# Performance work log

Hardware: AMD Instinct MI355X
Metric: run time of the kernel (lower is better)

## Reference

```python
import jax, jax.numpy as jnp
import numpy as np
import math

N_EMBD = 1024
NUM_HEADS = 16
HEAD_DIM = N_EMBD // NUM_HEADS


def alibi_slopes(num_heads):
    x = (2 ** 8) ** (1.0 / num_heads)
    return jnp.array([1.0 / x ** (i + 1) for i in range(num_heads)], dtype=jnp.float32)


def setup_inputs() -> dict:
    key = jax.random.key(0)
    k1, k2 = jax.random.split(key)
    x = jax.random.normal(k1, (2, 2048, N_EMBD), dtype=jnp.float32)
    W_kqv = jax.random.normal(k2, (3 * N_EMBD, N_EMBD), dtype=jnp.float32) * (1.0 / math.sqrt(N_EMBD))
    return {"x": x, "W_kqv": W_kqv}


def reference(x, W_kqv):
    B, S, E = x.shape
    H, D = NUM_HEADS, HEAD_DIM
    kqv = jnp.einsum('bse,fe->bsf', x, W_kqv)  # Linear without bias
    k, q, v = jnp.split(kqv, 3, axis=-1)       # chunk order: key, query, value
    # [B, H, S, D]
    q = q.reshape(B, S, H, D).transpose(0, 2, 1, 3)
    k = k.reshape(B, S, H, D).transpose(0, 2, 1, 3)
    v = v.reshape(B, S, H, D).transpose(0, 2, 1, 3)
    # ALiBi bias: slopes[h] * (j - i), shape [H, S, S]
    rel = jnp.arange(S)[None, :] - jnp.arange(S)[:, None]  # [S, S]
    bias = alibi_slopes(H)[:, None, None] * rel.astype(jnp.float32)
    scale = math.sqrt(E)  # NOTE: module scales by sqrt(n_embd), not sqrt(head_dim)
    score = jnp.einsum('bhqd,bhkd->bhqk', q, k) / scale + bias[None]
    causal = jnp.tril(jnp.ones((S, S), dtype=bool))
    score = jnp.where(causal[None, None], score, -jnp.inf)
    attn = jax.nn.softmax(score, axis=-1)
    out = jnp.einsum('bhqk,bhkd->bhqd', attn, v)
    return out.transpose(0, 2, 1, 3).reshape(B, S, E)
```

## Files before the change

### kernel.cpp

```cpp
#include <hip/hip_runtime.h>
#include <hip/hip_bf16.h>
#include <math.h>

#define TOTAL_B 2
#define SEQ 2048
#define EMB 1024
#define NH 16
#define HD 64
#define M_GEMM (TOTAL_B*SEQ)
#define N_GEMM (3*EMB)
#define K_GEMM EMB

typedef __attribute__((ext_vector_type(8))) short short8;
typedef __attribute__((ext_vector_type(4))) float f32x4;
typedef __attribute__((ext_vector_type(4))) unsigned u32x4;

static __device__ __forceinline__ short f2bf(float f) {
  union { float f; unsigned u; } v; v.f = f;
  unsigned r = v.u + 0x7fff + ((v.u >> 16) & 1u);
  return (short)(r >> 16);
}

static __device__ __forceinline__ void gload_lds16(const void* g, void* l) {
  __builtin_amdgcn_global_load_lds(
      (const __attribute__((address_space(1))) void*)(uintptr_t)g,
      (__attribute__((address_space(3))) void*)(uintptr_t)l, 16, 0, 0);
}

static __device__ __forceinline__ float exp2v(float x) {
  float r; asm("v_exp_f32 %0, %1" : "=v"(r) : "v"(x)); return r;
}
static __device__ __forceinline__ unsigned cvtpk(float lo, float hi) {
  unsigned r; asm("v_cvt_pk_bf16_f32 %0, %1, %2" : "=v"(r) : "v"(lo), "v"(hi)); return r;
}
static __device__ __forceinline__ void pl32swap(unsigned &a, unsigned &b) {
  asm("v_permlane32_swap_b32 %0, %1" : "+v"(a), "+v"(b));
}

__global__ void cvt_kernel(const float* __restrict__ x, const float* __restrict__ w,
                           short* __restrict__ xb, short* __restrict__ wb) {
  const long nx = (long)M_GEMM * K_GEMM;
  const long nw = (long)N_GEMM * K_GEMM;
  long i = (long)blockIdx.x * blockDim.x + threadIdx.x;
  const long tot = (nx + nw) / 8;
  if (i >= tot) return;
  long e = i * 8;
  const float* s; short* d;
  if (e < nx) { s = x + e; d = xb + e; }
  else        { s = w + (e - nx); d = wb + (e - nx); }
  float4 a = ((const float4*)s)[0];
  float4 b = ((const float4*)s)[1];
  short8 o;
  o[0]=f2bf(a.x); o[1]=f2bf(a.y); o[2]=f2bf(a.z); o[3]=f2bf(a.w);
  o[4]=f2bf(b.x); o[5]=f2bf(b.y); o[6]=f2bf(b.z); o[7]=f2bf(b.w);
  *(short8*)d = o;
}

__global__ __launch_bounds__(512, 2) void qkv_gemm(const short* __restrict__ A, const short* __restrict__ Bm,
                                                   short* __restrict__ Kb, short* __restrict__ Qb,
                                                   short* __restrict__ Vb) {
  __shared__ __align__(16) short lds[57344];
  const int tid = threadIdx.x;
  const int lane = tid & 63;
  const int wid = tid >> 6;
  const int lr = lane & 15, lg = lane >> 4;
  const int m0 = blockIdx.y * 256, n0 = blockIdx.x * 192;
  const int wr = wid >> 1;
  const int wc = wid & 1;
  const int srcRow = tid >> 3;
  const int srcCh  = (tid & 7) ^ (srcRow & 7);

  f32x4 acc[4][6] = {};

  auto stageA = [&](int buf, int kt, int u) {
    const int row = u*64 + srcRow;
    gload_lds16(A + (size_t)(m0 + row)*K_GEMM + kt*64 + srcCh*8,
                &lds[buf*16384 + u*4096 + tid*8]);
  };
  auto stageB = [&](int buf, int kt, int u) {
    const int row = u*64 + srcRow;
    gload_lds16(Bm + (size_t)(n0 + row)*K_GEMM + kt*64 + srcCh*8,
                &lds[32768 + buf*12288 + u*4096 + tid*8]);
  };
  auto readA = [&](int buf, int mi, int kk) -> short8 {
    const int r = wr*64 + mi*16 + lr;
    const int c = (kk*4 + lg) ^ (r & 7);
    return *(const short8*)(&lds[buf*16384 + r*64 + c*8]);
  };
  auto readB = [&](int buf, int nj, int kk) -> short8 {
    const int r = wc*96 + nj*16 + lr;
    const int c = (kk*4 + lg) ^ (r & 7);
    return *(const short8*)(&lds[32768 + buf*12288 + r*64 + c*8]);
  };

#pragma unroll
  for (int u = 0; u < 4; ++u) stageA(0, 0, u);
#pragma unroll
  for (int u = 0; u < 3; ++u) stageB(0, 0, u);
  asm volatile("s_waitcnt vmcnt(0)" ::: "memory");
  __builtin_amdgcn_s_barrier();

  short8 aq[2][2], bq[6][2];
  const int NT = K_GEMM / 64;
#pragma unroll 1
  for (int kt = 0; kt < NT; ++kt) {
    const int buf = kt & 1, nb = buf ^ 1;
    const bool more = (kt + 1 < NT);

#pragma unroll
    for (int kk = 0; kk < 2; ++kk) {
      aq[0][kk] = readA(buf, 0, kk); aq[1][kk] = readA(buf, 1, kk);
      bq[0][kk] = readB(buf, 0, kk); bq[1][kk] = readB(buf, 1, kk); bq[2][kk] = readB(buf, 2, kk);
    }
    if (more) { stageA(nb, kt+1, 0); stageA(nb, kt+1, 1); }
    __builtin_amdgcn_s_barrier();
    asm volatile("s_waitcnt lgkmcnt(0)" ::: "memory");
    __builtin_amdgcn_sched_barrier(0);
    __builtin_amdgcn_s_setprio(1);
#pragma unroll
    for (int mi = 0; mi < 2; ++mi)
#pragma unroll
      for (int nj = 0; nj < 3; ++nj)
#pragma unroll
        for (int kk = 0; kk < 2; ++kk)
          acc[mi][nj] = __builtin_amdgcn_mfma_f32_16x16x32_bf16(aq[mi][kk], bq[nj][kk], acc[mi][nj], 0, 0, 0);
    __builtin_amdgcn_s_setprio(0);
    __builtin_amdgcn_sched_barrier(0);
    __builtin_amdgcn_s_barrier();

#pragma unroll
    for (int kk = 0; kk < 2; ++kk) {
      bq[3][kk] = readB(buf, 3, kk); bq[4][kk] = readB(buf, 4, kk); bq[5][kk] = readB(buf, 5, kk);
    }
    if (more) { stageA(nb, kt+1, 2); stageA(nb, kt+1, 3); }
    __builtin_amdgcn_s_barrier();
    asm volatile("s_waitcnt lgkmcnt(0)" ::: "memory");
    __builtin_amdgcn_sched_barrier(0);
    __builtin_amdgcn_s_setprio(1);
#pragma unroll
    for (int mi = 0; mi < 2; ++mi)
#pragma unroll
      for (int nj = 3; nj < 6; ++nj)
#pragma unroll
        for (int kk = 0; kk < 2; ++kk)
          acc[mi][nj] = __builtin_amdgcn_mfma_f32_16x16x32_bf16(aq[mi][kk], bq[nj][kk], acc[mi][nj], 0, 0, 0);
    __builtin_amdgcn_s_setprio(0);
    __builtin_amdgcn_sched_barrier(0);
    __builtin_amdgcn_s_barrier();

#pragma unroll
    for (int kk = 0; kk < 2; ++kk) {
      aq[0][kk] = readA(buf, 2, kk); aq[1][kk] = readA(buf, 3, kk);
    }
    if (more) { stageB(nb, kt+1, 0); stageB(nb, kt+1, 1); }
    __builtin_amdgcn_s_barrier();
    asm volatile("s_waitcnt lgkmcnt(0)" ::: "memory");
    __builtin_amdgcn_sched_barrier(0);
    __builtin_amdgcn_s_setprio(1);
#pragma unroll
    for (int mi = 0; mi < 2; ++mi)
#pragma unroll
      for (int nj = 3; nj < 6; ++nj)
#pragma unroll
        for (int kk = 0; kk < 2; ++kk)
          acc[mi+2][nj] = __builtin_amdgcn_mfma_f32_16x16x32_bf16(aq[mi][kk], bq[nj][kk], acc[mi+2][nj], 0, 0, 0);
    __builtin_amdgcn_s_setprio(0);
    __builtin_amdgcn_sched_barrier(0);
    __builtin_amdgcn_s_barrier();

#pragma unroll
    for (int kk = 0; kk < 2; ++kk) {
      bq[0][kk] = readB(buf, 0, kk); bq[1][kk] = readB(buf, 1, kk); bq[2][kk] = readB(buf, 2, kk);
    }
    if (more) { stageB(nb, kt+1, 2); }
    __builtin_amdgcn_s_barrier();
    asm volatile("s_waitcnt lgkmcnt(0)" ::: "memory");
    __builtin_amdgcn_sched_barrier(0);
    __builtin_amdgcn_s_setprio(1);
#pragma unroll
    for (int mi = 0; mi < 2; ++mi)
#pragma unroll
      for (int nj = 0; nj < 3; ++nj)
#pragma unroll
        for (int kk = 0; kk < 2; ++kk)
          acc[mi+2][nj] = __builtin_amdgcn_mfma_f32_16x16x32_bf16(aq[mi][kk], bq[nj][kk], acc[mi+2][nj], 0, 0, 0);
    __builtin_amdgcn_s_setprio(0);
    __builtin_amdgcn_sched_barrier(0);

    asm volatile("s_waitcnt vmcnt(0)" ::: "memory");
    __builtin_amdgcn_s_barrier();
  }

#pragma unroll
  for (int nj = 0; nj < 6; ++nj) {
    const int f = n0 + wc*96 + nj*16 + lr;
    const int which = f >> 10, fl = f & 1023;
    const int h = fl >> 6, d = fl & 63;
    short* dst = (which == 0) ? Kb : (which == 1) ? Qb : Vb;
    const float scale = (which == 1) ? 0.04508422f : 1.0f;
    short* base = dst + (size_t)h*SEQ*HD + d;
#pragma unroll
    for (int mi = 0; mi < 4; ++mi)
#pragma unroll
      for (int r = 0; r < 4; ++r) {
        const int m = m0 + wr*64 + mi*16 + lg*4 + r;
        const int b = m >> 11, s = m & 2047;
        base[((size_t)b*NH*SEQ + s)*HD] = f2bf(acc[mi][nj][r] * scale);
      }
  }
}

__global__ void vtrans(const short* __restrict__ Vb, short* __restrict__ Vt) {
  __shared__ short t[64][72];
  const int hb = blockIdx.y;
  const int s0 = blockIdx.x * 64;
  const short* src = Vb + ((size_t)hb*SEQ + s0)*HD;
  short* dst = Vt + (size_t)hb*HD*SEQ;
  const int tid = threadIdx.x;
#pragma unroll
  for (int i = 0; i < 2; ++i) {
    const int e = i*2048 + tid*8;
    const int r = e >> 6, c = e & 63;
    short8 v = *(const short8*)(src + (size_t)r*HD + c);
#pragma unroll
    for (int j = 0; j < 8; ++j) t[r][c+j] = v[j];
  }
  __syncthreads();
#pragma unroll
  for (int i = 0; i < 2; ++i) {
    const int e = i*2048 + tid*8;
    const int d = e >> 6, ss = e & 63;
    short8 v;
#pragma unroll
    for (int j = 0; j < 8; ++j) v[j] = t[ss+j][d];
    *(short8*)(dst + (size_t)d*SEQ + s0 + ss) = v;
  }
}

__global__ __launch_bounds__(256, 4) void attn_kernel(const short* __restrict__ Kb, const short* __restrict__ Qb,
                                                      const short* __restrict__ Vt, float* __restrict__ Out,
                                                      float* __restrict__ Po, float2* __restrict__ Ml) {
  __shared__ __align__(16) short Ks[2][64*64];
  __shared__ __align__(16) short Vs[2][64*64];
  const int tid = threadIdx.x, lane = tid & 63, wid = tid >> 6;
  const int lr = lane & 15, lg = lane >> 4;
  const int bh = blockIdx.x;
  const int b = bh >> 4, h = bh & 15;
  const int y = blockIdx.y;
  int qt, t0, t1, part;
  if (y < 16) { qt = y; t0 = 0; t1 = qt + 1; part = -1; }
  else {
    const int p = (y - 16) >> 1;
    part = (y - 16) & 1;
    qt = 16 + p;
    const int hh = (qt + 1) >> 1;
    t0 = part ? hh : 0;
    t1 = part ? qt + 1 : hh;
  }
  const float slope = exp2f(-0.5f * (float)(h + 1)) * 1.44269504f;
  const short* Kp = Kb + (size_t)bh * SEQ * HD;
  const short* Qp = Qb + (size_t)bh * SEQ * HD;
  const short* Vp = Vt + (size_t)bh * HD * SEQ;
  float* Ob = Out + (size_t)b * SEQ * EMB + (size_t)h * HD;

  const int q0 = qt * 64, qrb = q0 + wid * 16;

  short8 qf[2];
#pragma unroll
  for (int kk = 0; kk < 2; ++kk)
    qf[kk] = *(const short8*)(Qp + (size_t)(qrb + lr)*HD + kk*32 + lg*8);

  const int bp = ((lr & 4) << 1) | ((lr & 2) << 1) | ((lr & 8) >> 2) | (lr & 1);
  const int cbase = qrb + lr - ((lg & 1) * 8 + (lg >> 1) * 2);

  float m_run = -INFINITY, l_run = 0.f;
  f32x4 o[4] = {};

  auto stageK = [&](int buf, int t) {
    const int kv0 = t * 64;
#pragma unroll
    for (int ii = 0; ii < 2; ++ii) {
      const int e16 = ii*256 + tid;
      const int row = e16 >> 3, ch = e16 & 7;
      const int sch = ch ^ (row & 7);
      gload_lds16(Kp + (size_t)(kv0 + row)*HD + sch*8, &Ks[buf][ii*2048 + wid*512]);
    }
  };
  auto stageV = [&](int buf, int t) {
    const int kv0 = t * 64;
#pragma unroll
    for (int ii = 0; ii < 2; ++ii) {
      const int e16 = ii*256 + tid;
      const int row = e16 >> 3, ch = e16 & 7;
      const int sch = ch ^ (row & 7);
      gload_lds16(Vp + (size_t)row*SEQ + kv0 + sch*8, &Vs[buf][ii*2048 + wid*512]);
    }
  };
  auto qkt = [&](int buf, f32x4* sc) {
    short8 kf[4][2];
#pragma unroll
    for (int kvf = 0; kvf < 4; ++kvf) {
      const int row = kvf*16 + bp;
#pragma unroll
      for (int kk = 0; kk < 2; ++kk) {
        const int c = (kk*4 + lg) ^ (row & 7);
        kf[kvf][kk] = *(const short8*)(&Ks[buf][row*64 + c*8]);
      }
    }
    __builtin_amdgcn_s_setprio(1);
#pragma unroll
    for (int kvf = 0; kvf < 4; ++kvf) {
      f32x4 s = {};
      s = __builtin_amdgcn_mfma_f32_16x16x32_bf16(kf[kvf][0], qf[0], s, 0, 0, 0);
      s = __builtin_amdgcn_mfma_f32_16x16x32_bf16(kf[kvf][1], qf[1], s, 0, 0, 0);
      sc[kvf] = s;
    }
    __builtin_amdgcn_s_setprio(0);
  };
  auto biasmax = [&](int tt, const f32x4* sc, float vv[4][4]) -> float {
    const float dbase = (float)(tt*64 - cbase);
    if (tt == qt) {
#pragma unroll
      for (int kvf = 0; kvf < 4; ++kvf)
#pragma unroll
        for (int r = 0; r < 4; ++r) {
          const float C = (float)(kvf*16 + (r>>1)*4 + (r&1));
          const float toff = dbase + C;
          float val = fmaf(slope, toff, sc[kvf][r]);
          if (toff > 0.f) val = -INFINITY;
          vv[kvf][r] = val;
        }
    } else {
#pragma unroll
      for (int kvf = 0; kvf < 4; ++kvf)
#pragma unroll
        for (int r = 0; r < 4; ++r) {
          const float C = (float)(kvf*16 + (r>>1)*4 + (r&1));
          vv[kvf][r] = fmaf(slope, dbase + C, sc[kvf][r]);
        }
    }
    float a0 = fmaxf(fmaxf(vv[0][0], vv[0][1]), fmaxf(vv[0][2], vv[0][3]));
    float a1 = fmaxf(fmaxf(vv[1][0], vv[1][1]), fmaxf(vv[1][2], vv[1][3]));
    float a2 = fmaxf(fmaxf(vv[2][0], vv[2][1]), fmaxf(vv[2][2], vv[2][3]));
    float a3 = fmaxf(fmaxf(vv[3][0], vv[3][1]), fmaxf(vv[3][2], vv[3][3]));
    float mt = fmaxf(fmaxf(a0, a1), fmaxf(a2, a3));
    mt = fmaxf(mt, __shfl_xor(mt, 16, 64));
    mt = fmaxf(mt, __shfl_xor(mt, 32, 64));
    return mt;
  };

  stageK(0, t0);
  if (t1 - t0 > 1) stageK(1, t0 + 1);
  stageV(0, t0);
  __syncthreads();
  f32x4 sc[4];
  qkt(0, sc);
  float vc[4][4];
  m_run = biasmax(t0, sc, vc);
  __syncthreads();

#pragma unroll 1
  for (int t = t0; t < t1; ++t) {
    const int u = t - t0;
    if (t + 1 < t1) stageV((u + 1) & 1, t + 1);
    if (t + 2 < t1) stageK(u & 1, t + 2);

    float vn[4][4];
    const bool have_next = (t + 1 < t1);
    if (have_next) {
      qkt((u + 1) & 1, sc);
      const float mtn = biasmax(t + 1, sc, vn);
      if (__any(mtn > m_run + 10.f)) {
        const float mn = fmaxf(m_run, mtn);
        const float corr = exp2v(m_run - mn);
        m_run = mn;
        l_run *= corr;
        float co[4];
#pragma unroll
        for (int r = 0; r < 4; ++r) co[r] = __shfl(corr, lg*4 + r, 64);
#pragma unroll
        for (int dt = 0; dt < 4; ++dt)
#pragma unroll
          for (int r = 0; r < 4; ++r) o[dt][r] *= co[r];
      }
    }

#pragma unroll
    for (int kvf = 0; kvf < 4; ++kvf)
#pragma unroll
      for (int r = 0; r < 4; ++r)
        vc[kvf][r] = exp2v(vc[kvf][r] - m_run);
    float s0 = (vc[0][0]+vc[0][1]) + (vc[0][2]+vc[0][3]);
    float s1 = (vc[1][0]+vc[1][1]) + (vc[1][2]+vc[1][3]);
    float s2 = (vc[2][0]+vc[2][1]) + (vc[2][2]+vc[2][3]);
    float s3 = (vc[3][0]+vc[3][1]) + (vc[3][2]+vc[3][3]);
    float lt = (s0+s1) + (s2+s3);
    lt += __shfl_xor(lt, 16, 64);
    lt += __shfl_xor(lt, 32, 64);
    l_run += lt;

    unsigned pk[4][2];
#pragma unroll
    for (int kvf = 0; kvf < 4; ++kvf) {
      pk[kvf][0] = cvtpk(vc[kvf][0], vc[kvf][1]);
      pk[kvf][1] = cvtpk(vc[kvf][2], vc[kvf][3]);
    }
    __builtin_amdgcn_s_setprio(1);
#pragma unroll
    for (int ks = 0; ks < 2; ++ks) {
      unsigned w0 = pk[2*ks][0], w1 = pk[2*ks+1][0];
      pl32swap(w0, w1);
      unsigned w2 = pk[2*ks][1], w3 = pk[2*ks+1][1];
      pl32swap(w2, w3);
      u32x4 wv = {w0, w1, w2, w3};
      const short8 pf = __builtin_bit_cast(short8, wv);
#pragma unroll
      for (int dt = 0; dt < 4; ++dt) {
        const int rv = dt*16 + lr;
        const int cv = (ks*4 + lg) ^ (rv & 7);
        const short8 vf = *(const short8*)(&Vs[u & 1][rv*64 + cv*8]);
        o[dt] = __builtin_amdgcn_mfma_f32_16x16x32_bf16(pf, vf, o[dt], 0, 0, 0);
      }
    }
    __builtin_amdgcn_s_setprio(0);

    __syncthreads();
    if (have_next) {
#pragma unroll
      for (int kvf = 0; kvf < 4; ++kvf)
#pragma unroll
        for (int r = 0; r < 4; ++r)
          vc[kvf][r] = vn[kvf][r];
    }
  }

  if (part < 0) {
    const float inv = 1.f / l_run;
    float li[4];
#pragma unroll
    for (int r = 0; r < 4; ++r) li[r] = __shfl(inv, lg*4 + r, 64);
#pragma unroll
    for (int dt = 0; dt < 4; ++dt)
#pragma unroll
      for (int r = 0; r < 4; ++r) {
        const int iq = qrb + lg*4 + r;
        Ob[(size_t)iq*EMB + dt*16 + lr] = o[dt][r] * li[r];
      }
  } else {
    const int pidx = bh * 16 + (qt - 16);
    if (lg == 0) Ml[(size_t)(pidx*2 + part)*64 + wid*16 + lr] = make_float2(m_run, l_run);
    if (part == 0) {
#pragma unroll
      for (int dt = 0; dt < 4; ++dt)
#pragma unroll
        for (int r = 0; r < 4; ++r) {
          const int iq = qrb + lg*4 + r;
          Ob[(size_t)iq*EMB + dt*16 + lr] = o[dt][r];
        }
    } else {
      float* pp = Po + (size_t)pidx*4096;
#pragma unroll
      for (int dt = 0; dt < 4; ++dt)
#pragma unroll
        for (int r = 0; r < 4; ++r) {
          const int ql = wid*16 + lg*4 + r;
          pp[ql*64 + dt*16 + lr] = o[dt][r];
        }
    }
  }
}

__global__ __launch_bounds__(256) void combine_kernel(const float* __restrict__ Po, const float2* __restrict__ Ml,
                                                      float* __restrict__ Out) {
  const int qi = blockIdx.x;
  const int bh = blockIdx.y;
  const int pidx = bh*16 + qi;
  const int qt = 16 + qi;
  const int b = bh >> 4, h = bh & 15;
  const int tid = threadIdx.x;
  const int row = tid >> 2;
  const int c0 = (tid & 3) * 16;
  const float2 ml0 = Ml[(size_t)(pidx*2 + 0)*64 + row];
  const float2 ml1 = Ml[(size_t)(pidx*2 + 1)*64 + row];
  const float m = fmaxf(ml0.x, ml1.x);
  const float e0 = exp2f(ml0.x - m), e1 = exp2f(ml1.x - m);
  const float l = ml0.y*e0 + ml1.y*e1;
  const float sc0 = e0 / l, sc1 = e1 / l;
  const int q = qt*64 + row;
  float* op = Out + (size_t)b*SEQ*EMB + (size_t)q*EMB + h*HD + c0;
  const float* pp = Po + (size_t)pidx*4096 + row*64 + c0;
#pragma unroll
  for (int i = 0; i < 4; ++i) {
    float4 a = ((const float4*)op)[i];
    float4 c = ((const float4*)pp)[i];
    float4 r;
    r.x = a.x*sc0 + c.x*sc1;
    r.y = a.y*sc0 + c.y*sc1;
    r.z = a.z*sc0 + c.z*sc1;
    r.w = a.w*sc0 + c.w*sc1;
    ((float4*)op)[i] = r;
  }
}

extern "C" void kernel_launch(void* const* d_in, const int* in_sizes, int n_in,
                              void* d_out, int out_size, void* d_ws, size_t ws_size,
                              hipStream_t stream) {
  const float* x = (const float*)d_in[0];
  const float* w = (const float*)d_in[1];
  char* ws = (char*)d_ws;
  if (ws_size < 39845888u) return;
  short* xb = (short*)(ws);
  short* wb = (short*)(ws + 8388608u);
  short* Kb = (short*)(ws + 14680064u);
  short* Qb = (short*)(ws + 23068672u);
  short* Vb = (short*)(ws + 31457280u);
  short* Vt = xb;
  float2* Ml = (float2*)(ws + 8388608u);
  float*  Po = (float*)(ws + 31457280u);
  float* out = (float*)d_out;

  cvt_kernel<<<3584, 256, 0, stream>>>(x, w, xb, wb);
  qkv_gemm<<<dim3(N_GEMM/192, M_GEMM/256), 512, 0, stream>>>(xb, wb, Kb, Qb, Vb);
  vtrans<<<dim3(SEQ/64, TOTAL_B*NH), 256, 0, stream>>>(Vb, Vt);
  attn_kernel<<<dim3(TOTAL_B*NH, 48), 256, 0, stream>>>(Kb, Qb, Vt, out, Po, Ml);
  combine_kernel<<<dim3(16, TOTAL_B*NH), 256, 0, stream>>>(Po, Ml, out);
}
```

Baseline: 102.2 us.

## Process 128 query rows per attention block with triple-buffered K tiles

Each attention block now covers 128 query rows, with every wave holding two 16-row Q fragments, so each K/V tile loaded into LDS feeds twice as many MFMAs. The one-tile-ahead QK^T software pipeline is replaced by a triple-buffered K ring synchronised with explicit vmcnt waits and raw barriers. The grid shrinks to 24 y-blocks and the split-KV combine is reworked for the 128-row tiles. The trade-off is higher register pressure (launch bounds drop to 3 waves), fewer blocks to fill the GPU, and the loss of overlap between QK^T and softmax.

```diff
diff --git a/kernel.cpp b/kernel.cpp
--- a/kernel.cpp
+++ b/kernel.cpp
@@ -237,44 +237,51 @@
   }
 }
 
-__global__ __launch_bounds__(256, 4) void attn_kernel(const short* __restrict__ Kb, const short* __restrict__ Qb,
+__global__ __launch_bounds__(256, 3) void attn_kernel(const short* __restrict__ Kb, const short* __restrict__ Qb,
                                                       const short* __restrict__ Vt, float* __restrict__ Out,
                                                       float* __restrict__ Po, float2* __restrict__ Ml) {
-  __shared__ __align__(16) short Ks[2][64*64];
+  __shared__ __align__(16) short Ks[3][64*64];
   __shared__ __align__(16) short Vs[2][64*64];
   const int tid = threadIdx.x, lane = tid & 63, wid = tid >> 6;
   const int lr = lane & 15, lg = lane >> 4;
   const int bh = blockIdx.x;
   const int b = bh >> 4, h = bh & 15;
   const int y = blockIdx.y;
-  int qt, t0, t1, part;
-  if (y < 16) { qt = y; t0 = 0; t1 = qt + 1; part = -1; }
+  int j, t0, t1, part;
+  if (y < 8) { j = y; part = -1; t0 = 0; t1 = 2*j + 2; }
   else {
-    const int p = (y - 16) >> 1;
-    part = (y - 16) & 1;
-    qt = 16 + p;
-    const int hh = (qt + 1) >> 1;
+    const int p = (y - 8) >> 1;
+    part = (y - 8) & 1;
+    j = 8 + p;
+    const int hh = j + 1;
     t0 = part ? hh : 0;
-    t1 = part ? qt + 1 : hh;
-  }
+    t1 = part ? 2*j + 2 : hh;
+  }
+  const int diag0 = 2*j;
   const float slope = exp2f(-0.5f * (float)(h + 1)) * 1.44269504f;
   const short* Kp = Kb + (size_t)bh * SEQ * HD;
   const short* Qp = Qb + (size_t)bh * SEQ * HD;
   const short* Vp = Vt + (size_t)bh * HD * SEQ;
   float* Ob = Out + (size_t)b * SEQ * EMB + (size_t)h * HD;
 
-  const int q0 = qt * 64, qrb = q0 + wid * 16;
-
-  short8 qf[2];
-#pragma unroll
-  for (int kk = 0; kk < 2; ++kk)
-    qf[kk] = *(const short8*)(Qp + (size_t)(qrb + lr)*HD + kk*32 + lg*8);
+  const int q0 = j * 128;
+  const int qrb0 = q0 + wid * 32;
+
+  short8 qf[2][2];
+#pragma unroll
+  for (int qi = 0; qi < 2; ++qi)
+#pragma unroll
+    for (int kk = 0; kk < 2; ++kk)
+      qf[qi][kk] = *(const short8*)(Qp + (size_t)(qrb0 + qi*16 + lr)*HD + kk*32 + lg*8);
 
   const int bp = ((lr & 4) << 1) | ((lr & 2) << 1) | ((lr & 8) >> 2) | (lr & 1);
-  const int cbase = qrb + lr - ((lg & 1) * 8 + (lg >> 1) * 2);
-
-  float m_run = -INFINITY, l_run = 0.f;
-  f32x4 o[4] = {};
+  int cb[2];
+#pragma unroll
+  for (int qi = 0; qi < 2; ++qi)
+    cb[qi] = qrb0 + qi*16 + lr - ((lg & 1) * 8 + (lg >> 1) * 2);
+
+  float m_run[2] = {-INFINITY, -INFINITY}, l_run[2] = {0.f, 0.f};
+  f32x4 o[2][4] = {};
 
   auto stageK = [&](int buf, int t) {
     const int kv0 = t * 64;
@@ -296,201 +303,210 @@
       gload_lds16(Vp + (size_t)row*SEQ + kv0 + sch*8, &Vs[buf][ii*2048 + wid*512]);
     }
   };
-  auto qkt = [&](int buf, f32x4* sc) {
-    short8 kf[4][2];
-#pragma unroll
-    for (int kvf = 0; kvf < 4; ++kvf) {
-      const int row = kvf*16 + bp;
-#pragma unroll
-      for (int kk = 0; kk < 2; ++kk) {
-        const int c = (kk*4 + lg) ^ (row & 7);
-        kf[kvf][kk] = *(const short8*)(&Ks[buf][row*64 + c*8]);
-      }
-    }
-    __builtin_amdgcn_s_setprio(1);
-#pragma unroll
-    for (int kvf = 0; kvf < 4; ++kvf) {
-      f32x4 s = {};
-      s = __builtin_amdgcn_mfma_f32_16x16x32_bf16(kf[kvf][0], qf[0], s, 0, 0, 0);
-      s = __builtin_amdgcn_mfma_f32_16x16x32_bf16(kf[kvf][1], qf[1], s, 0, 0, 0);
-      sc[kvf] = s;
-    }
-    __builtin_amdgcn_s_setprio(0);
-  };
-  auto biasmax = [&](int tt, const f32x4* sc, float vv[4][4]) -> float {
-    const float dbase = (float)(tt*64 - cbase);
-    if (tt == qt) {
-#pragma unroll
-      for (int kvf = 0; kvf < 4; ++kvf)
-#pragma unroll
-        for (int r = 0; r < 4; ++r) {
-          const float C = (float)(kvf*16 + (r>>1)*4 + (r&1));
-          const float toff = dbase + C;
-          float val = fmaf(slope, toff, sc[kvf][r]);
-          if (toff > 0.f) val = -INFINITY;
-          vv[kvf][r] = val;
-        }
-    } else {
-#pragma unroll
-      for (int kvf = 0; kvf < 4; ++kvf)
-#pragma unroll
-        for (int r = 0; r < 4; ++r) {
-          const float C = (float)(kvf*16 + (r>>1)*4 + (r&1));
-          vv[kvf][r] = fmaf(slope, dbase + C, sc[kvf][r]);
-        }
-    }
-    float a0 = fmaxf(fmaxf(vv[0][0], vv[0][1]), fmaxf(vv[0][2], vv[0][3]));
-    float a1 = fmaxf(fmaxf(vv[1][0], vv[1][1]), fmaxf(vv[1][2], vv[1][3]));
-    float a2 = fmaxf(fmaxf(vv[2][0], vv[2][1]), fmaxf(vv[2][2], vv[2][3]));
-    float a3 = fmaxf(fmaxf(vv[3][0], vv[3][1]), fmaxf(vv[3][2], vv[3][3]));
-    float mt = fmaxf(fmaxf(a0, a1), fmaxf(a2, a3));
-    mt = fmaxf(mt, __shfl_xor(mt, 16, 64));
-    mt = fmaxf(mt, __shfl_xor(mt, 32, 64));
-    return mt;
-  };
 
   stageK(0, t0);
-  if (t1 - t0 > 1) stageK(1, t0 + 1);
+  stageK(1, t0 + 1);
   stageV(0, t0);
-  __syncthreads();
-  f32x4 sc[4];
-  qkt(0, sc);
-  float vc[4][4];
-  m_run = biasmax(t0, sc, vc);
-  __syncthreads();
+  asm volatile("s_waitcnt vmcnt(0)" ::: "memory");
+  __builtin_amdgcn_s_barrier();
 
 #pragma unroll 1
   for (int t = t0; t < t1; ++t) {
     const int u = t - t0;
     if (t + 1 < t1) stageV((u + 1) & 1, t + 1);
-    if (t + 2 < t1) stageK(u & 1, t + 2);
-
-    float vn[4][4];
-    const bool have_next = (t + 1 < t1);
-    if (have_next) {
-      qkt((u + 1) & 1, sc);
-      const float mtn = biasmax(t + 1, sc, vn);
-      if (__any(mtn > m_run + 10.f)) {
-        const float mn = fmaxf(m_run, mtn);
-        const float corr = exp2v(m_run - mn);
-        m_run = mn;
-        l_run *= corr;
+    const bool moreK = (t + 2 < t1);
+    if (moreK) stageK((u + 2) % 3, t + 2);
+
+    const short* Kbuf = &Ks[u % 3][0];
+    short8 kf[4][2];
+#pragma unroll
+    for (int kvf = 0; kvf < 4; ++kvf) {
+      const int row = kvf*16 + bp;
+#pragma unroll
+      for (int kk = 0; kk < 2; ++kk) {
+        const int c = (kk*4 + lg) ^ (row & 7);
+        kf[kvf][kk] = *(const short8*)(Kbuf + row*64 + c*8);
+      }
+    }
+    f32x4 sc[2][4];
+    __builtin_amdgcn_s_setprio(1);
+#pragma unroll
+    for (int qi = 0; qi < 2; ++qi)
+#pragma unroll
+      for (int kvf = 0; kvf < 4; ++kvf) {
+        f32x4 s = {};
+        s = __builtin_amdgcn_mfma_f32_16x16x32_bf16(kf[kvf][0], qf[qi][0], s, 0, 0, 0);
+        s = __builtin_amdgcn_mfma_f32_16x16x32_bf16(kf[kvf][1], qf[qi][1], s, 0, 0, 0);
+        sc[qi][kvf] = s;
+      }
+    __builtin_amdgcn_s_setprio(0);
+
+    const bool needMask = (t >= diag0);
+    float vv[2][4][4];
+    float mt[2];
+#pragma unroll
+    for (int qi = 0; qi < 2; ++qi) {
+      const float dbase = (float)(t*64 - cb[qi]);
+#pragma unroll
+      for (int kvf = 0; kvf < 4; ++kvf)
+#pragma unroll
+        for (int r = 0; r < 4; ++r) {
+          const float C = (float)(kvf*16 + (r>>1)*4 + (r&1));
+          const float toff = dbase + C;
+          float val = fmaf(slope, toff, sc[qi][kvf][r]);
+          if (needMask && toff > 0.f) val = -INFINITY;
+          vv[qi][kvf][r] = val;
+        }
+      float a0 = fmaxf(fmaxf(vv[qi][0][0], vv[qi][0][1]), fmaxf(vv[qi][0][2], vv[qi][0][3]));
+      float a1 = fmaxf(fmaxf(vv[qi][1][0], vv[qi][1][1]), fmaxf(vv[qi][1][2], vv[qi][1][3]));
+      float a2 = fmaxf(fmaxf(vv[qi][2][0], vv[qi][2][1]), fmaxf(vv[qi][2][2], vv[qi][2][3]));
+      float a3 = fmaxf(fmaxf(vv[qi][3][0], vv[qi][3][1]), fmaxf(vv[qi][3][2], vv[qi][3][3]));
+      float m = fmaxf(fmaxf(a0, a1), fmaxf(a2, a3));
+      m = fmaxf(m, __shfl_xor(m, 16, 64));
+      m = fmaxf(m, __shfl_xor(m, 32, 64));
+      mt[qi] = m;
+    }
+
+    if (__any(mt[0] > m_run[0] + 10.f) || __any(mt[1] > m_run[1] + 10.f)) {
+#pragma unroll
+      for (int qi = 0; qi < 2; ++qi) {
+        const float mn = fmaxf(m_run[qi], mt[qi]);
+        const float corr = exp2v(m_run[qi] - mn);
+        m_run[qi] = mn;
+        l_run[qi] *= corr;
         float co[4];
 #pragma unroll
         for (int r = 0; r < 4; ++r) co[r] = __shfl(corr, lg*4 + r, 64);
 #pragma unroll
         for (int dt = 0; dt < 4; ++dt)
 #pragma unroll
-          for (int r = 0; r < 4; ++r) o[dt][r] *= co[r];
-      }
-    }
-
-#pragma unroll
-    for (int kvf = 0; kvf < 4; ++kvf)
-#pragma unroll
-      for (int r = 0; r < 4; ++r)
-        vc[kvf][r] = exp2v(vc[kvf][r] - m_run);
-    float s0 = (vc[0][0]+vc[0][1]) + (vc[0][2]+vc[0][3]);
-    float s1 = (vc[1][0]+vc[1][1]) + (vc[1][2]+vc[1][3]);
-    float s2 = (vc[2][0]+vc[2][1]) + (vc[2][2]+vc[2][3]);
-    float s3 = (vc[3][0]+vc[3][1]) + (vc[3][2]+vc[3][3]);
-    float lt = (s0+s1) + (s2+s3);
-    lt += __shfl_xor(lt, 16, 64);
-    lt += __shfl_xor(lt, 32, 64);
-    l_run += lt;
-
-    unsigned pk[4][2];
-#pragma unroll
-    for (int kvf = 0; kvf < 4; ++kvf) {
-      pk[kvf][0] = cvtpk(vc[kvf][0], vc[kvf][1]);
-      pk[kvf][1] = cvtpk(vc[kvf][2], vc[kvf][3]);
-    }
+          for (int r = 0; r < 4; ++r) o[qi][dt][r] *= co[r];
+      }
+    }
+
+#pragma unroll
+    for (int qi = 0; qi < 2; ++qi) {
+#pragma unroll
+      for (int kvf = 0; kvf < 4; ++kvf)
+#pragma unroll
+        for (int r = 0; r < 4; ++r)
+          vv[qi][kvf][r] = exp2v(vv[qi][kvf][r] - m_run[qi]);
+      float s0 = (vv[qi][0][0]+vv[qi][0][1]) + (vv[qi][0][2]+vv[qi][0][3]);
+      float s1 = (vv[qi][1][0]+vv[qi][1][1]) + (vv[qi][1][2]+vv[qi][1][3]);
+      float s2 = (vv[qi][2][0]+vv[qi][2][1]) + (vv[qi][2][2]+vv[qi][2][3]);
+      float s3 = (vv[qi][3][0]+vv[qi][3][1]) + (vv[qi][3][2]+vv[qi][3][3]);
+      float lt = (s0+s1) + (s2+s3);
+      lt += __shfl_xor(lt, 16, 64);
+      lt += __shfl_xor(lt, 32, 64);
+      l_run[qi] += lt;
+    }
+
+    unsigned pk[2][4][2];
+#pragma unroll
+    for (int qi = 0; qi < 2; ++qi)
+#pragma unroll
+      for (int kvf = 0; kvf < 4; ++kvf) {
+        pk[qi][kvf][0] = cvtpk(vv[qi][kvf][0], vv[qi][kvf][1]);
+        pk[qi][kvf][1] = cvtpk(vv[qi][kvf][2], vv[qi][kvf][3]);
+      }
+
+    const short* Vbuf = &Vs[u & 1][0];
     __builtin_amdgcn_s_setprio(1);
 #pragma unroll
     for (int ks = 0; ks < 2; ++ks) {
-      unsigned w0 = pk[2*ks][0], w1 = pk[2*ks+1][0];
-      pl32swap(w0, w1);
-      unsigned w2 = pk[2*ks][1], w3 = pk[2*ks+1][1];
-      pl32swap(w2, w3);
-      u32x4 wv = {w0, w1, w2, w3};
-      const short8 pf = __builtin_bit_cast(short8, wv);
+      short8 pf[2];
+#pragma unroll
+      for (int qi = 0; qi < 2; ++qi) {
+        unsigned w0 = pk[qi][2*ks][0], w1 = pk[qi][2*ks+1][0];
+        pl32swap(w0, w1);
+        unsigned w2 = pk[qi][2*ks][1], w3 = pk[qi][2*ks+1][1];
+        pl32swap(w2, w3);
+        u32x4 wv = {w0, w1, w2, w3};
+        pf[qi] = __builtin_bit_cast(short8, wv);
+      }
 #pragma unroll
       for (int dt = 0; dt < 4; ++dt) {
         const int rv = dt*16 + lr;
         const int cv = (ks*4 + lg) ^ (rv & 7);
-        const short8 vf = *(const short8*)(&Vs[u & 1][rv*64 + cv*8]);
-        o[dt] = __builtin_amdgcn_mfma_f32_16x16x32_bf16(pf, vf, o[dt], 0, 0, 0);
+        const short8 vf = *(const short8*)(Vbuf + rv*64 + cv*8);
+        o[0][dt] = __builtin_amdgcn_mfma_f32_16x16x32_bf16(pf[0], vf, o[0][dt], 0, 0, 0);
+        o[1][dt] = __builtin_amdgcn_mfma_f32_16x16x32_bf16(pf[1], vf, o[1][dt], 0, 0, 0);
       }
     }
     __builtin_amdgcn_s_setprio(0);
 
-    __syncthreads();
-    if (have_next) {
-#pragma unroll
-      for (int kvf = 0; kvf < 4; ++kvf)
-#pragma unroll
-        for (int r = 0; r < 4; ++r)
-          vc[kvf][r] = vn[kvf][r];
-    }
+    if (moreK) asm volatile("s_waitcnt vmcnt(2) lgkmcnt(0)" ::: "memory");
+    else       asm volatile("s_waitcnt vmcnt(0) lgkmcnt(0)" ::: "memory");
+    __builtin_amdgcn_s_barrier();
   }
 
   if (part < 0) {
-    const float inv = 1.f / l_run;
-    float li[4];
-#pragma unroll
-    for (int r = 0; r < 4; ++r) li[r] = __shfl(inv, lg*4 + r, 64);
-#pragma unroll
-    for (int dt = 0; dt < 4; ++dt)
-#pragma unroll
-      for (int r = 0; r < 4; ++r) {
-        const int iq = qrb + lg*4 + r;
-        Ob[(size_t)iq*EMB + dt*16 + lr] = o[dt][r] * li[r];
-      }
+#pragma unroll
+    for (int qi = 0; qi < 2; ++qi) {
+      const float inv = 1.f / l_run[qi];
+      float li[4];
+#pragma unroll
+      for (int r = 0; r < 4; ++r) li[r] = __shfl(inv, lg*4 + r, 64);
+#pragma unroll
+      for (int dt = 0; dt < 4; ++dt)
+#pragma unroll
+        for (int r = 0; r < 4; ++r) {
+          const int iq = qrb0 + qi*16 + lg*4 + r;
+          Ob[(size_t)iq*EMB + dt*16 + lr] = o[qi][dt][r] * li[r];
+        }
+    }
   } else {
-    const int pidx = bh * 16 + (qt - 16);
-    if (lg == 0) Ml[(size_t)(pidx*2 + part)*64 + wid*16 + lr] = make_float2(m_run, l_run);
+    const int pidx = bh * 8 + (j - 8);
+    if (lg == 0) {
+#pragma unroll
+      for (int qi = 0; qi < 2; ++qi)
+        Ml[(size_t)(pidx*2 + part)*128 + wid*32 + qi*16 + lr] = make_float2(m_run[qi], l_run[qi]);
+    }
     if (part == 0) {
 #pragma unroll
-      for (int dt = 0; dt < 4; ++dt)
-#pragma unroll
-        for (int r = 0; r < 4; ++r) {
-          const int iq = qrb + lg*4 + r;
-          Ob[(size_t)iq*EMB + dt*16 + lr] = o[dt][r];
-        }
+      for (int qi = 0; qi < 2; ++qi)
+#pragma unroll
+        for (int dt = 0; dt < 4; ++dt)
+#pragma unroll
+          for (int r = 0; r < 4; ++r) {
+            const int iq = qrb0 + qi*16 + lg*4 + r;
+            Ob[(size_t)iq*EMB + dt*16 + lr] = o[qi][dt][r];
+          }
     } else {
-      float* pp = Po + (size_t)pidx*4096;
-#pragma unroll
-      for (int dt = 0; dt < 4; ++dt)
-#pragma unroll
-        for (int r = 0; r < 4; ++r) {
-          const int ql = wid*16 + lg*4 + r;
-          pp[ql*64 + dt*16 + lr] = o[dt][r];
-        }
+      float* pp = Po + (size_t)pidx*8192;
+#pragma unroll
+      for (int qi = 0; qi < 2; ++qi)
+#pragma unroll
+        for (int dt = 0; dt < 4; ++dt)
+#pragma unroll
+          for (int r = 0; r < 4; ++r) {
+            const int ql = wid*32 + qi*16 + lg*4 + r;
+            pp[ql*64 + dt*16 + lr] = o[qi][dt][r];
+          }
     }
   }
 }
 
 __global__ __launch_bounds__(256) void combine_kernel(const float* __restrict__ Po, const float2* __restrict__ Ml,
                                                       float* __restrict__ Out) {
-  const int qi = blockIdx.x;
+  const int ji = blockIdx.x;
   const int bh = blockIdx.y;
-  const int pidx = bh*16 + qi;
-  const int qt = 16 + qi;
+  const int pidx = bh*8 + ji;
   const int b = bh >> 4, h = bh & 15;
   const int tid = threadIdx.x;
-  const int row = tid >> 2;
-  const int c0 = (tid & 3) * 16;
-  const float2 ml0 = Ml[(size_t)(pidx*2 + 0)*64 + row];
-  const float2 ml1 = Ml[(size_t)(pidx*2 + 1)*64 + row];
+  const int row = tid >> 1;
+  const int half = tid & 1;
+  const float2 ml0 = Ml[(size_t)(pidx*2 + 0)*128 + row];
+  const float2 ml1 = Ml[(size_t)(pidx*2 + 1)*128 + row];
   const float m = fmaxf(ml0.x, ml1.x);
   const float e0 = exp2f(ml0.x - m), e1 = exp2f(ml1.x - m);
   const float l = ml0.y*e0 + ml1.y*e1;
   const float sc0 = e0 / l, sc1 = e1 / l;
-  const int q = qt*64 + row;
-  float* op = Out + (size_t)b*SEQ*EMB + (size_t)q*EMB + h*HD + c0;
-  const float* pp = Po + (size_t)pidx*4096 + row*64 + c0;
-#pragma unroll
-  for (int i = 0; i < 4; ++i) {
+  const int q = (8 + ji)*128 + row;
+  float* op = Out + (size_t)b*SEQ*EMB + (size_t)q*EMB + h*HD + half*32;
+  const float* pp = Po + (size_t)pidx*8192 + row*64 + half*32;
+#pragma unroll
+  for (int i = 0; i < 8; ++i) {
     float4 a = ((const float4*)op)[i];
     float4 c = ((const float4*)pp)[i];
     float4 r;
@@ -522,6 +538,6 @@
   cvt_kernel<<<3584, 256, 0, stream>>>(x, w, xb, wb);
   qkv_gemm<<<dim3(N_GEMM/192, M_GEMM/256), 512, 0, stream>>>(xb, wb, Kb, Qb, Vb);
   vtrans<<<dim3(SEQ/64, TOTAL_B*NH), 256, 0, stream>>>(Vb, Vt);
-  attn_kernel<<<dim3(TOTAL_B*NH, 48), 256, 0, stream>>>(Kb, Qb, Vt, out, Po, Ml);
-  combine_kernel<<<dim3(16, TOTAL_B*NH), 256, 0, stream>>>(Po, Ml, out);
-}
+  attn_kernel<<<dim3(TOTAL_B*NH, 24), 256, 0, stream>>>(Kb, Qb, Vt, out, Po, Ml);
+  combine_kernel<<<dim3(8, TOTAL_B*NH), 256, 0, stream>>>(Po, Ml, out);
+}
```

Result: slower. 108.0 us (+5.7%).

## Split all query tiles into two KV halves, read V from global directly

Applied to the files above, without the earlier changes.

Every query tile is now split into two KV-range halves, giving a uniform 64-way grid instead of 16 whole tiles plus split tiles, and every tile goes through the combine kernel. V is no longer staged through LDS but read straight from global memory (the transposed layout) inside the PV MFMA loop. That halves shared memory and raises the occupancy hint to 8 blocks. Partial outputs are stored as bf16 to cut workspace traffic, at some precision cost and with more global-latency exposure on V reads.

```diff
diff --git a/kernel.cpp b/kernel.cpp
--- a/kernel.cpp
+++ b/kernel.cpp
@@ -19,6 +19,9 @@
   union { float f; unsigned u; } v; v.f = f;
   unsigned r = v.u + 0x7fff + ((v.u >> 16) & 1u);
   return (short)(r >> 16);
+}
+static __device__ __forceinline__ float bf2f(unsigned short s) {
+  union { unsigned u; float f; } v; v.u = ((unsigned)s) << 16; return v.f;
 }
 
 static __device__ __forceinline__ void gload_lds16(const void* g, void* l) {
@@ -237,26 +240,20 @@
   }
 }
 
-__global__ __launch_bounds__(256, 4) void attn_kernel(const short* __restrict__ Kb, const short* __restrict__ Qb,
+__global__ __launch_bounds__(256, 8) void attn_kernel(const short* __restrict__ Kb, const short* __restrict__ Qb,
                                                       const short* __restrict__ Vt, float* __restrict__ Out,
-                                                      float* __restrict__ Po, float2* __restrict__ Ml) {
+                                                      short* __restrict__ Po, float2* __restrict__ Ml) {
   __shared__ __align__(16) short Ks[2][64*64];
-  __shared__ __align__(16) short Vs[2][64*64];
   const int tid = threadIdx.x, lane = tid & 63, wid = tid >> 6;
   const int lr = lane & 15, lg = lane >> 4;
   const int bh = blockIdx.x;
   const int b = bh >> 4, h = bh & 15;
   const int y = blockIdx.y;
-  int qt, t0, t1, part;
-  if (y < 16) { qt = y; t0 = 0; t1 = qt + 1; part = -1; }
-  else {
-    const int p = (y - 16) >> 1;
-    part = (y - 16) & 1;
-    qt = 16 + p;
-    const int hh = (qt + 1) >> 1;
-    t0 = part ? hh : 0;
-    t1 = part ? qt + 1 : hh;
-  }
+  const int part = y & 1, qt = y >> 1;
+  const int nt = qt + 1;
+  const int hh = (nt + 1) >> 1;
+  const int t0 = part ? hh : 0;
+  const int t1 = part ? nt : hh;
   const float slope = exp2f(-0.5f * (float)(h + 1)) * 1.44269504f;
   const short* Kp = Kb + (size_t)bh * SEQ * HD;
   const short* Qp = Qb + (size_t)bh * SEQ * HD;
@@ -264,11 +261,6 @@
   float* Ob = Out + (size_t)b * SEQ * EMB + (size_t)h * HD;
 
   const int q0 = qt * 64, qrb = q0 + wid * 16;
-
-  short8 qf[2];
-#pragma unroll
-  for (int kk = 0; kk < 2; ++kk)
-    qf[kk] = *(const short8*)(Qp + (size_t)(qrb + lr)*HD + kk*32 + lg*8);
 
   const int bp = ((lr & 4) << 1) | ((lr & 2) << 1) | ((lr & 8) >> 2) | (lr & 1);
   const int cbase = qrb + lr - ((lg & 1) * 8 + (lg >> 1) * 2);
@@ -286,196 +278,177 @@
       gload_lds16(Kp + (size_t)(kv0 + row)*HD + sch*8, &Ks[buf][ii*2048 + wid*512]);
     }
   };
-  auto stageV = [&](int buf, int t) {
-    const int kv0 = t * 64;
-#pragma unroll
-    for (int ii = 0; ii < 2; ++ii) {
-      const int e16 = ii*256 + tid;
-      const int row = e16 >> 3, ch = e16 & 7;
-      const int sch = ch ^ (row & 7);
-      gload_lds16(Vp + (size_t)row*SEQ + kv0 + sch*8, &Vs[buf][ii*2048 + wid*512]);
+
+  if (t0 < t1) {
+    short8 qf[2];
+#pragma unroll
+    for (int kk = 0; kk < 2; ++kk)
+      qf[kk] = *(const short8*)(Qp + (size_t)(qrb + lr)*HD + kk*32 + lg*8);
+
+    auto qkt = [&](int buf, f32x4* sc) {
+      short8 kf[4][2];
+#pragma unroll
+      for (int kvf = 0; kvf < 4; ++kvf) {
+        const int row = kvf*16 + bp;
+#pragma unroll
+        for (int kk = 0; kk < 2; ++kk) {
+          const int c = (kk*4 + lg) ^ (row & 7);
+          kf[kvf][kk] = *(const short8*)(&Ks[buf][row*64 + c*8]);
+        }
+      }
+      __builtin_amdgcn_s_setprio(1);
+#pragma unroll
+      for (int kvf = 0; kvf < 4; ++kvf) {
+        f32x4 s = {};
+        s = __builtin_amdgcn_mfma_f32_16x16x32_bf16(kf[kvf][0], qf[0], s, 0, 0, 0);
+        s = __builtin_amdgcn_mfma_f32_16x16x32_bf16(kf[kvf][1], qf[1], s, 0, 0, 0);
+        sc[kvf] = s;
+      }
+      __builtin_amdgcn_s_setprio(0);
+    };
+    auto biasmax = [&](int tt, const f32x4* sc, float vv[4][4]) -> float {
+      const float dbase = (float)(tt*64 - cbase);
+      if (tt == qt) {
+#pragma unroll
+        for (int kvf = 0; kvf < 4; ++kvf)
+#pragma unroll
+          for (int r = 0; r < 4; ++r) {
+            const float C = (float)(kvf*16 + (r>>1)*4 + (r&1));
+            const float toff = dbase + C;
+            float val = fmaf(slope, toff, sc[kvf][r]);
+            if (toff > 0.f) val = -INFINITY;
+            vv[kvf][r] = val;
+          }
+      } else {
+#pragma unroll
+        for (int kvf = 0; kvf < 4; ++kvf)
+#pragma unroll
+          for (int r = 0; r < 4; ++r) {
+            const float C = (float)(kvf*16 + (r>>1)*4 + (r&1));
+            vv[kvf][r] = fmaf(slope, dbase + C, sc[kvf][r]);
+          }
+      }
+      float a0 = fmaxf(fmaxf(vv[0][0], vv[0][1]), fmaxf(vv[0][2], vv[0][3]));
+      float a1 = fmaxf(fmaxf(vv[1][0], vv[1][1]), fmaxf(vv[1][2], vv[1][3]));
+      float a2 = fmaxf(fmaxf(vv[2][0], vv[2][1]), fmaxf(vv[2][2], vv[2][3]));
+      float a3 = fmaxf(fmaxf(vv[3][0], vv[3][1]), fmaxf(vv[3][2], vv[3][3]));
+      float mt = fmaxf(fmaxf(a0, a1), fmaxf(a2, a3));
+      mt = fmaxf(mt, __shfl_xor(mt, 16, 64));
+      mt = fmaxf(mt, __shfl_xor(mt, 32, 64));
+      return mt;
+    };
+
+    stageK(0, t0);
+    if (t1 - t0 > 1) stageK(1, t0 + 1);
+    asm volatile("s_waitcnt vmcnt(0)" ::: "memory");
+    __syncthreads();
+    f32x4 sc[4];
+    qkt(0, sc);
+    float vc[4][4];
+    m_run = biasmax(t0, sc, vc);
+    __syncthreads();
+
+#pragma unroll 1
+    for (int t = t0; t < t1; ++t) {
+      const int u = t - t0;
+      if (t + 2 < t1) stageK(u & 1, t + 2);
+
+      float vn[4][4];
+      const bool have_next = (t + 1 < t1);
+      if (have_next) {
+        qkt((u + 1) & 1, sc);
+        const float mtn = biasmax(t + 1, sc, vn);
+        if (__any(mtn > m_run + 10.f)) {
+          const float mn = fmaxf(m_run, mtn);
+          const float corr = exp2v(m_run - mn);
+          m_run = mn;
+          l_run *= corr;
+          float co[4];
+#pragma unroll
+          for (int r = 0; r < 4; ++r) co[r] = __shfl(corr, lg*4 + r, 64);
+#pragma unroll
+          for (int dt = 0; dt < 4; ++dt)
+#pragma unroll
+            for (int r = 0; r < 4; ++r) o[dt][r] *= co[r];
+        }
+      }
+
+#pragma unroll
+      for (int kvf = 0; kvf < 4; ++kvf)
+#pragma unroll
+        for (int r = 0; r < 4; ++r)
+          vc[kvf][r] = exp2v(vc[kvf][r] - m_run);
+      float s0 = (vc[0][0]+vc[0][1]) + (vc[0][2]+vc[0][3]);
+      float s1 = (vc[1][0]+vc[1][1]) + (vc[1][2]+vc[1][3]);
+      float s2 = (vc[2][0]+vc[2][1]) + (vc[2][2]+vc[2][3]);
+      float s3 = (vc[3][0]+vc[3][1]) + (vc[3][2]+vc[3][3]);
+      float lt = (s0+s1) + (s2+s3);
+      lt += __shfl_xor(lt, 16, 64);
+      lt += __shfl_xor(lt, 32, 64);
+      l_run += lt;
+
+      unsigned pk[4][2];
+#pragma unroll
+      for (int kvf = 0; kvf < 4; ++kvf) {
+        pk[kvf][0] = cvtpk(vc[kvf][0], vc[kvf][1]);
+        pk[kvf][1] = cvtpk(vc[kvf][2], vc[kvf][3]);
+      }
+      const short* Vb0 = Vp + t*64 + lg*8;
+      __builtin_amdgcn_s_setprio(1);
+#pragma unroll
+      for (int ks = 0; ks < 2; ++ks) {
+        unsigned w0 = pk[2*ks][0], w1 = pk[2*ks+1][0];
+        pl32swap(w0, w1);
+        unsigned w2 = pk[2*ks][1], w3 = pk[2*ks+1][1];
+        pl32swap(w2, w3);
+        u32x4 wv = {w0, w1, w2, w3};
+        const short8 pf = __builtin_bit_cast(short8, wv);
+#pragma unroll
+        for (int dt = 0; dt < 4; ++dt) {
+          const short8 vf = *(const short8*)(Vb0 + (size_t)(dt*16 + lr)*SEQ + ks*32);
+          o[dt] = __builtin_amdgcn_mfma_f32_16x16x32_bf16(pf, vf, o[dt], 0, 0, 0);
+        }
+      }
+      __builtin_amdgcn_s_setprio(0);
+
+      __syncthreads();
+      if (have_next) {
+#pragma unroll
+        for (int kvf = 0; kvf < 4; ++kvf)
+#pragma unroll
+          for (int r = 0; r < 4; ++r)
+            vc[kvf][r] = vn[kvf][r];
+      }
     }
-  };
-  auto qkt = [&](int buf, f32x4* sc) {
-    short8 kf[4][2];
-#pragma unroll
-    for (int kvf = 0; kvf < 4; ++kvf) {
-      const int row = kvf*16 + bp;
-#pragma unroll
-      for (int kk = 0; kk < 2; ++kk) {
-        const int c = (kk*4 + lg) ^ (row & 7);
-        kf[kvf][kk] = *(const short8*)(&Ks[buf][row*64 + c*8]);
-      }
-    }
-    __builtin_amdgcn_s_setprio(1);
-#pragma unroll
-    for (int kvf = 0; kvf < 4; ++kvf) {
-      f32x4 s = {};
-      s = __builtin_amdgcn_mfma_f32_16x16x32_bf16(kf[kvf][0], qf[0], s, 0, 0, 0);
-      s = __builtin_amdgcn_mfma_f32_16x16x32_bf16(kf[kvf][1], qf[1], s, 0, 0, 0);
-      sc[kvf] = s;
-    }
-    __builtin_amdgcn_s_setprio(0);
-  };
-  auto biasmax = [&](int tt, const f32x4* sc, float vv[4][4]) -> float {
-    const float dbase = (float)(tt*64 - cbase);
-    if (tt == qt) {
-#pragma unroll
-      for (int kvf = 0; kvf < 4; ++kvf)
-#pragma unroll
-        for (int r = 0; r < 4; ++r) {
-          const float C = (float)(kvf*16 + (r>>1)*4 + (r&1));
-          const float toff = dbase + C;
-          float val = fmaf(slope, toff, sc[kvf][r]);
-          if (toff > 0.f) val = -INFINITY;
-          vv[kvf][r] = val;
-        }
-    } else {
-#pragma unroll
-      for (int kvf = 0; kvf < 4; ++kvf)
-#pragma unroll
-        for (int r = 0; r < 4; ++r) {
-          const float C = (float)(kvf*16 + (r>>1)*4 + (r&1));
-          vv[kvf][r] = fmaf(slope, dbase + C, sc[kvf][r]);
-        }
-    }
-    float a0 = fmaxf(fmaxf(vv[0][0], vv[0][1]), fmaxf(vv[0][2], vv[0][3]));
-    float a1 = fmaxf(fmaxf(vv[1][0], vv[1][1]), fmaxf(vv[1][2], vv[1][3]));
-    float a2 = fmaxf(fmaxf(vv[2][0], vv[2][1]), fmaxf(vv[2][2], vv[2][3]));
-    float a3 = fmaxf(fmaxf(vv[3][0], vv[3][1]), fmaxf(vv[3][2], vv[3][3]));
-    float mt = fmaxf(fmaxf(a0, a1), fmaxf(a2, a3));
-    mt = fmaxf(mt, __shfl_xor(mt, 16, 64));
-    mt = fmaxf(mt, __shfl_xor(mt, 32, 64));
-    return mt;
-  };
-
-  stageK(0, t0);
-  if (t1 - t0 > 1) stageK(1, t0 + 1);
-  stageV(0, t0);
-  __syncthreads();
-  f32x4 sc[4];
-  qkt(0, sc);
-  float vc[4][4];
-  m_run = biasmax(t0, sc, vc);
-  __syncthreads();
-
-#pragma unroll 1
-  for (int t = t0; t < t1; ++t) {
-    const int u = t - t0;
-    if (t + 1 < t1) stageV((u + 1) & 1, t + 1);
-    if (t + 2 < t1) stageK(u & 1, t + 2);
-
-    float vn[4][4];
-    const bool have_next = (t + 1 < t1);
-    if (have_next) {
-      qkt((u + 1) & 1, sc);
-      const float mtn = biasmax(t + 1, sc, vn);
-      if (__any(mtn > m_run + 10.f)) {
-        const float mn = fmaxf(m_run, mtn);
-        const float corr = exp2v(m_run - mn);
-        m_run = mn;
-        l_run *= corr;
-        float co[4];
-#pragma unroll
-        for (int r = 0; r < 4; ++r) co[r] = __shfl(corr, lg*4 + r, 64);
-#pragma unroll
-        for (int dt = 0; dt < 4; ++dt)
-#pragma unroll
-          for (int r = 0; r < 4; ++r) o[dt][r] *= co[r];
-      }
-    }
-
-#pragma unroll
-    for (int kvf = 0; kvf < 4; ++kvf)
-#pragma unroll
-      for (int r = 0; r < 4; ++r)
-        vc[kvf][r] = exp2v(vc[kvf][r] - m_run);
-    float s0 = (vc[0][0]+vc[0][1]) + (vc[0][2]+vc[0][3]);
-    float s1 = (vc[1][0]+vc[1][1]) + (vc[1][2]+vc[1][3]);
-    float s2 = (vc[2][0]+vc[2][1]) + (vc[2][2]+vc[2][3]);
-    float s3 = (vc[3][0]+vc[3][1]) + (vc[3][2]+vc[3][3]);
-    float lt = (s0+s1) + (s2+s3);
-    lt += __shfl_xor(lt, 16, 64);
-    lt += __shfl_xor(lt, 32, 64);
-    l_run += lt;
-
-    unsigned pk[4][2];
-#pragma unroll
-    for (int kvf = 0; kvf < 4; ++kvf) {
-      pk[kvf][0] = cvtpk(vc[kvf][0], vc[kvf][1]);
-      pk[kvf][1] = cvtpk(vc[kvf][2], vc[kvf][3]);
-    }
-    __builtin_amdgcn_s_setprio(1);
-#pragma unroll
-    for (int ks = 0; ks < 2; ++ks) {
-      unsigned w0 = pk[2*ks][0], w1 = pk[2*ks+1][0];
-      pl32swap(w0, w1);
-      unsigned w2 = pk[2*ks][1], w3 = pk[2*ks+1][1];
-      pl32swap(w2, w3);
-      u32x4 wv = {w0, w1, w2, w3};
-      const short8 pf = __builtin_bit_cast(short8, wv);
-#pragma unroll
-      for (int dt = 0; dt < 4; ++dt) {
-        const int rv = dt*16 + lr;
-        const int cv = (ks*4 + lg) ^ (rv & 7);
-        const short8 vf = *(const short8*)(&Vs[u & 1][rv*64 + cv*8]);
-        o[dt] = __builtin_amdgcn_mfma_f32_16x16x32_bf16(pf, vf, o[dt], 0, 0, 0);
-      }
-    }
-    __builtin_amdgcn_s_setprio(0);
-
-    __syncthreads();
-    if (have_next) {
-#pragma unroll
-      for (int kvf = 0; kvf < 4; ++kvf)
-#pragma unroll
-        for (int r = 0; r < 4; ++r)
-          vc[kvf][r] = vn[kvf][r];
-    }
-  }
-
-  if (part < 0) {
-    const float inv = 1.f / l_run;
-    float li[4];
-#pragma unroll
-    for (int r = 0; r < 4; ++r) li[r] = __shfl(inv, lg*4 + r, 64);
+  }
+
+  const int pidx = bh * 32 + qt;
+  if (lg == 0) Ml[(size_t)(pidx*2 + part)*64 + wid*16 + lr] = make_float2(m_run, l_run);
+  if (part == 0) {
 #pragma unroll
     for (int dt = 0; dt < 4; ++dt)
 #pragma unroll
       for (int r = 0; r < 4; ++r) {
         const int iq = qrb + lg*4 + r;
-        Ob[(size_t)iq*EMB + dt*16 + lr] = o[dt][r] * li[r];
+        Ob[(size_t)iq*EMB + dt*16 + lr] = o[dt][r];
       }
   } else {
-    const int pidx = bh * 16 + (qt - 16);
-    if (lg == 0) Ml[(size_t)(pidx*2 + part)*64 + wid*16 + lr] = make_float2(m_run, l_run);
-    if (part == 0) {
-#pragma unroll
-      for (int dt = 0; dt < 4; ++dt)
-#pragma unroll
-        for (int r = 0; r < 4; ++r) {
-          const int iq = qrb + lg*4 + r;
-          Ob[(size_t)iq*EMB + dt*16 + lr] = o[dt][r];
-        }
-    } else {
-      float* pp = Po + (size_t)pidx*4096;
-#pragma unroll
-      for (int dt = 0; dt < 4; ++dt)
-#pragma unroll
-        for (int r = 0; r < 4; ++r) {
-          const int ql = wid*16 + lg*4 + r;
-          pp[ql*64 + dt*16 + lr] = o[dt][r];
-        }
-    }
-  }
-}
-
-__global__ __launch_bounds__(256) void combine_kernel(const float* __restrict__ Po, const float2* __restrict__ Ml,
+    short* pp = Po + (size_t)pidx*4096;
+#pragma unroll
+    for (int dt = 0; dt < 4; ++dt)
+#pragma unroll
+      for (int r = 0; r < 4; ++r) {
+        const int ql = wid*16 + lg*4 + r;
+        pp[ql*64 + dt*16 + lr] = f2bf(o[dt][r]);
+      }
+  }
+}
+
+__global__ __launch_bounds__(256) void combine_kernel(const short* __restrict__ Po, const float2* __restrict__ Ml,
                                                       float* __restrict__ Out) {
-  const int qi = blockIdx.x;
+  const int qt = blockIdx.x;
   const int bh = blockIdx.y;
-  const int pidx = bh*16 + qi;
-  const int qt = 16 + qi;
+  const int pidx = bh*32 + qt;
   const int b = bh >> 4, h = bh & 15;
   const int tid = threadIdx.x;
   const int row = tid >> 2;
@@ -488,16 +461,16 @@
   const float sc0 = e0 / l, sc1 = e1 / l;
   const int q = qt*64 + row;
   float* op = Out + (size_t)b*SEQ*EMB + (size_t)q*EMB + h*HD + c0;
-  const float* pp = Po + (size_t)pidx*4096 + row*64 + c0;
+  const short* pp = Po + (size_t)pidx*4096 + row*64 + c0;
 #pragma unroll
   for (int i = 0; i < 4; ++i) {
     float4 a = ((const float4*)op)[i];
-    float4 c = ((const float4*)pp)[i];
+    short4 c4 = ((const short4*)pp)[i];
     float4 r;
-    r.x = a.x*sc0 + c.x*sc1;
-    r.y = a.y*sc0 + c.y*sc1;
-    r.z = a.z*sc0 + c.z*sc1;
-    r.w = a.w*sc0 + c.w*sc1;
+    r.x = a.x*sc0 + bf2f((unsigned short)c4.x)*sc1;
+    r.y = a.y*sc0 + bf2f((unsigned short)c4.y)*sc1;
+    r.z = a.z*sc0 + bf2f((unsigned short)c4.z)*sc1;
+    r.w = a.w*sc0 + bf2f((unsigned short)c4.w)*sc1;
     ((float4*)op)[i] = r;
   }
 }
@@ -516,12 +489,12 @@
   short* Vb = (short*)(ws + 31457280u);
   short* Vt = xb;
   float2* Ml = (float2*)(ws + 8388608u);
-  float*  Po = (float*)(ws + 31457280u);
+  short*  Po = (short*)(ws + 31457280u);
   float* out = (float*)d_out;
 
   cvt_kernel<<<3584, 256, 0, stream>>>(x, w, xb, wb);
   qkv_gemm<<<dim3(N_GEMM/192, M_GEMM/256), 512, 0, stream>>>(xb, wb, Kb, Qb, Vb);
   vtrans<<<dim3(SEQ/64, TOTAL_B*NH), 256, 0, stream>>>(Vb, Vt);
-  attn_kernel<<<dim3(TOTAL_B*NH, 48), 256, 0, stream>>>(Kb, Qb, Vt, out, Po, Ml);
-  combine_kernel<<<dim3(16, TOTAL_B*NH), 256, 0, stream>>>(Po, Ml, out);
-}
+  attn_kernel<<<dim3(TOTAL_B*NH, 64), 256, 0, stream>>>(Kb, Qb, Vt, out, Po, Ml);
+  combine_kernel<<<dim3(32, TOTAL_B*NH), 256, 0, stream>>>(Po, Ml, out);
+}
```

Measured after the change: 315.5 us. +208.8%, slower.
